# Kernel optimization log

Measured on AMD Instinct MI355X. Metric: run time of the kernel, lower is better.

Reference implementation:

```python
import jax, jax.numpy as jnp
import numpy as np

WS = 7
SHIFT = 3
S_SIZE = 20.0
T_SIZE = 1.0
DIM = 256
HEADS = 8
EPS = 1e-5


def _rel_pos_index(ws):
    coords = np.stack(np.meshgrid(np.arange(ws), np.arange(ws), indexing='ij')).reshape(2, -1)
    rel = (coords[:, :, None] - coords[:, None, :]).transpose(1, 2, 0).copy()
    rel[..., 0] += ws - 1
    rel[..., 1] += ws - 1
    rel[..., 0] *= 2 * ws - 1
    return rel.sum(-1)  # (ws*ws, ws*ws)


def _calc_masks(H, W, ws, shift, s_size, t_size):
    # shifted-window mask (standard Swin)
    img = np.zeros((H, W), dtype=np.float32)
    sl = (slice(0, -ws), slice(-ws, -shift), slice(-shift, None))
    cnt = 0
    for h in sl:
        for w in sl:
            img[h, w] = cnt
            cnt += 1
    N = ws * ws
    mw = img.reshape(H // ws, ws, W // ws, ws).transpose(0, 2, 1, 3).reshape(-1, N)
    am = np.where((mw[:, None, :] - mw[:, :, None]) != 0, -100.0, 0.0).astype(np.float32)
    # physical 'cone' masks
    kmh = 1000.0 / 3600.0
    cv_min, cv_max = 60.0 * kmh, 100.0 * kmh
    cw_min, cw_max = 10.0 * kmh, 25.0 * kmh
    r = np.arange(ws)
    rr, cc = np.meshgrid(r, r, indexing='ij')
    coords = np.stack([rr.ravel(), cc.ravel()], -1)
    delta = coords[:, None, :] - coords[None, :, :]
    dy = delta[..., 0].astype(np.float32) * s_size
    dt = delta[..., 1].astype(np.float32) * t_size
    eye = np.eye(N, dtype=bool)
    dt_pos = dt > 0
    safe_dt = np.where(dt_pos, dt, 1.0)
    sp = np.where(dt_pos, dy / safe_dt, 0.0)
    allow_v = (dt_pos & (dy >= 0) & (sp >= cv_min) & (sp <= cv_max)) | eye
    cone_v = np.where(allow_v, 0.0, -100.0).astype(np.float32)
    spw = np.where(dt_pos, np.abs(dy) / safe_dt, 0.0)
    allow_w = (dt_pos & (dy <= 0) & (spw >= cw_min) & (spw <= cw_max)) | eye
    cone_w = np.where(allow_w, 0.0, -100.0).astype(np.float32)
    return am + cone_v[None], am + cone_w[None]


def _ln(x, g, b):
    mu = jnp.mean(x, -1, keepdims=True)
    var = jnp.mean((x - mu) ** 2, -1, keepdims=True)
    return (x - mu) / jnp.sqrt(var + EPS) * g + b


def _win_part(x, ws):
    B, H, W, C = x.shape
    return x.reshape(B, H // ws, ws, W // ws, ws, C).transpose(0, 1, 3, 2, 4, 5).reshape(-1, ws * ws, C)


def _win_rev(w, ws, H, W):
    B = w.shape[0] // ((H // ws) * (W // ws))
    return w.reshape(B, H // ws, W // ws, ws, ws, -1).transpose(0, 1, 3, 2, 4, 5).reshape(B, H, W, -1)


def _wattn(xw, qkv_w, qkv_b, proj_w, proj_b, rpb, mask, rpi, nH):
    Bw, N, Ch = xw.shape
    hd = Ch // nH
    qkv = (xw @ qkv_w.T + qkv_b).reshape(Bw, N, 3, nH, hd).transpose(2, 0, 3, 1, 4)
    q = qkv[0] * (hd ** -0.5)
    attn = jnp.einsum('bhnd,bhmd->bhnm', q, qkv[1])
    bias = rpb[rpi.reshape(-1)].reshape(N, N, nH).transpose(2, 0, 1)
    attn = attn + bias[None]
    nW = mask.shape[0]
    attn = (attn.reshape(Bw // nW, nW, nH, N, N) + mask[None, :, None]).reshape(Bw, nH, N, N)
    attn = jax.nn.softmax(attn, axis=-1)
    out = jnp.einsum('bhnm,bhmd->bhnd', attn, qkv[2]).transpose(0, 2, 1, 3).reshape(Bw, N, Ch)
    return out @ proj_w.T + proj_b


def _forward(H, W, x, norm1_g, norm1_b, norm2_g, norm2_b,
             qkv_w1, qkv_b1, proj_w1, proj_b1, rpb1,
             qkv_w2, qkv_b2, proj_w2, proj_b2, rpb2,
             fc1_w, fc1_b, fc2_w, fc2_b):
    B, L, C = x.shape
    ws, shift = WS, SHIFT
    m1, m2 = _calc_masks(H, W, ws, shift, S_SIZE, T_SIZE)
    m1, m2 = jnp.asarray(m1), jnp.asarray(m2)
    rpi = jnp.asarray(_rel_pos_index(ws))
    nH = HEADS // 2
    shortcut = x
    xn = _ln(x, norm1_g, norm1_b).reshape(B, H, W, C)
    halves = []
    for xh, qw, qb, pw, pb, rpb, m in (
        (xn[..., :C // 2], qkv_w1, qkv_b1, proj_w1, proj_b1, rpb1, m1),
        (xn[..., C // 2:], qkv_w2, qkv_b2, proj_w2, proj_b2, rpb2, m2),
    ):
        sx = jnp.roll(xh, (-shift, -shift), (1, 2))
        aw = _wattn(_win_part(sx, ws), qw, qb, pw, pb, rpb, m, rpi, nH)
        halves.append(jnp.roll(_win_rev(aw, ws, H, W), (shift, shift), (1, 2)))
    x = shortcut + jnp.concatenate(halves, -1).reshape(B, L, C)
    h = _ln(x, norm2_g, norm2_b)
    h = jax.nn.gelu(h @ fc1_w.T + fc1_b, approximate=False)
    return x + (h @ fc2_w.T + fc2_b)


def setup_inputs() -> dict:
    key = jax.random.key(0)
    B, H, W, C = 2, 224, 224, DIM
    Ch = C // 2
    hid = 4 * C
    nrpb = (2 * WS - 1) * (2 * WS - 1)
    nHh = HEADS // 2
    ks = jax.random.split(key, 16)
    p = lambda k, shape: 0.02 * jax.random.normal(k, shape, dtype=jnp.float32)
    return {
        'x': jax.random.normal(ks[0], (B, H * W, C), dtype=jnp.float32),
        'H': H, 'W': W,
        'norm1_g': jnp.ones((C,), jnp.float32), 'norm1_b': jnp.zeros((C,), jnp.float32),
        'norm2_g': jnp.ones((C,), jnp.float32), 'norm2_b': jnp.zeros((C,), jnp.float32),
        'qkv_w1': p(ks[1], (3 * Ch, Ch)), 'qkv_b1': jnp.zeros((3 * Ch,), jnp.float32),
        'proj_w1': p(ks[2], (Ch, Ch)), 'proj_b1': jnp.zeros((Ch,), jnp.float32),
        'rpb1': p(ks[3], (nrpb, nHh)),
        'qkv_w2': p(ks[4], (3 * Ch, Ch)), 'qkv_b2': jnp.zeros((3 * Ch,), jnp.float32),
        'proj_w2': p(ks[5], (Ch, Ch)), 'proj_b2': jnp.zeros((Ch,), jnp.float32),
        'rpb2': p(ks[6], (nrpb, nHh)),
        'fc1_w': p(ks[7], (hid, C)), 'fc1_b': jnp.zeros((hid,), jnp.float32),
        'fc2_w': p(ks[8], (C, hid)), 'fc2_b': jnp.zeros((C,), jnp.float32),
    }


def reference(x, H, W, norm1_g, norm1_b, norm2_g, norm2_b,
              qkv_w1, qkv_b1, proj_w1, proj_b1, rpb1,
              qkv_w2, qkv_b2, proj_w2, proj_b2, rpb2,
              fc1_w, fc1_b, fc2_w, fc2_b):
    return _forward(H, W, x, norm1_g, norm1_b, norm2_g, norm2_b,
                    qkv_w1, qkv_b1, proj_w1, proj_b1, rpb1,
                    qkv_w2, qkv_b2, proj_w2, proj_b2, rpb2,
                    fc1_w, fc1_b, fc2_w, fc2_b)
```

## Files before the change

### kernel.cpp

```cpp
#include <hip/hip_runtime.h>

using u16 = unsigned short;
typedef short short8 __attribute__((ext_vector_type(8)));
typedef float f32x4 __attribute__((ext_vector_type(4)));

#define T_TOK 100352

__device__ __forceinline__ float bf2f(u16 u) {
    return __uint_as_float(((unsigned int)u) << 16);
}
__device__ __forceinline__ u16 f2bf(float f) {
    unsigned int u = __float_as_uint(f);
    u += 0x7fffu + ((u >> 16) & 1u);
    return (u16)(u >> 16);
}

__global__ __launch_bounds__(256) void cvt_bf16_k(const float* __restrict__ src,
                                                  u16* __restrict__ dst, int n) {
    int i = blockIdx.x * 256 + threadIdx.x;
    int stride = gridDim.x * 256;
    for (; i < n; i += stride) dst[i] = f2bf(src[i]);
}

__global__ __launch_bounds__(256) void bias_tbl_k(const float* __restrict__ rpb0,
                                                  const float* __restrict__ rpb1,
                                                  float* __restrict__ tbl) {
    int id = blockIdx.x;
    int hsel = id >> 4, wtype = (id >> 2) & 3, h = id & 3;
    const float* rpb = hsel ? rpb1 : rpb0;
    int redge = wtype >> 1, cedge = wtype & 1;
    float* o = tbl + (size_t)id * 2401;
    for (int i = threadIdx.x; i < 2401; i += 256) {
        int n = i / 49, m = i - n * 49;
        int rn = n / 7, cn = n - rn * 7, rm = m / 7, cm = m - rm * 7;
        int rpi = (rn - rm + 6) * 13 + (cn - cm + 6);
        float v = rpb[rpi * 4 + h];
        int grn = redge ? (rn < 4 ? 1 : 2) : 0;
        int grm = redge ? (rm < 4 ? 1 : 2) : 0;
        int gcn = cedge ? (cn < 4 ? 1 : 2) : 0;
        int gcm = cedge ? (cm < 4 ? 1 : 2) : 0;
        if ((grn * 3 + gcn) != (grm * 3 + gcm)) v += -100.0f;
        int dr = rn - rm, dc = cn - cm;
        bool ok;
        if (n == m) ok = true;
        else if (hsel == 0)
            ok = (dc == 1 && dr == 1) || (dc == 2 && dr == 2) ||
                 (dc == 3 && (dr == 3 || dr == 4)) ||
                 (dc == 4 && (dr == 4 || dr == 5)) ||
                 (dc == 5 && (dr == 5 || dr == 6)) ||
                 (dc == 6 && (dr == 5 || dr == 6));
        else
            ok = (dr == -1 && dc >= 3 && dc <= 6) || (dr == -2 && dc == 6);
        if (!ok) v += -100.0f;
        o[i] = v;
    }
}

__global__ __launch_bounds__(256) void ln1_k(const float* __restrict__ x,
                                             const float* __restrict__ g,
                                             const float* __restrict__ b,
                                             u16* __restrict__ xw) {
    int t = blockIdx.x * 4 + (threadIdx.x >> 6);
    int lane = threadIdx.x & 63;
    const float4 v = *(const float4*)(x + (size_t)t * 256 + lane * 4);
    float s = v.x + v.y + v.z + v.w;
    float s2 = v.x * v.x + v.y * v.y + v.z * v.z + v.w * v.w;
#pragma unroll
    for (int off = 1; off < 64; off <<= 1) {
        s += __shfl_xor(s, off);
        s2 += __shfl_xor(s2, off);
    }
    float mean = s * (1.0f / 256.0f);
    float var = s2 * (1.0f / 256.0f) - mean * mean;
    float rstd = 1.0f / sqrtf(var + 1e-5f);

    int bb = (t >= 50176) ? 1 : 0;
    int l = t - bb * 50176;
    int rr = l / 224, cc = l - rr * 224;
    int r2 = rr - 3; if (r2 < 0) r2 += 224;
    int c2 = cc - 3; if (c2 < 0) c2 += 224;
    int wi = r2 / 7, lr = r2 - wi * 7;
    int wj = c2 / 7, lc = c2 - wj * 7;
    size_t mIdx = (size_t)(((bb << 10) + wi * 32 + wj) * 49 + lr * 7 + lc);

    int ch = lane * 4;
    int hsel = ch >> 7, colb = ch & 127;
    const float4 gv = *(const float4*)(g + ch);
    const float4 bv = *(const float4*)(b + ch);
    union { uint2 u; u16 s4[4]; } pk;
    pk.s4[0] = f2bf((v.x - mean) * rstd * gv.x + bv.x);
    pk.s4[1] = f2bf((v.y - mean) * rstd * gv.y + bv.y);
    pk.s4[2] = f2bf((v.z - mean) * rstd * gv.z + bv.z);
    pk.s4[3] = f2bf((v.w - mean) * rstd * gv.w + bv.w);
    *(uint2*)(xw + (size_t)hsel * T_TOK * 128 + mIdx * 128 + colb) = pk.u;
}

__global__ __launch_bounds__(256) void ln2_k(const float* __restrict__ x,
                                             const float* __restrict__ g,
                                             const float* __restrict__ b,
                                             u16* __restrict__ h) {
    int t = blockIdx.x * 4 + (threadIdx.x >> 6);
    int lane = threadIdx.x & 63;
    const float4 v = *(const float4*)(x + (size_t)t * 256 + lane * 4);
    float s = v.x + v.y + v.z + v.w;
    float s2 = v.x * v.x + v.y * v.y + v.z * v.z + v.w * v.w;
#pragma unroll
    for (int off = 1; off < 64; off <<= 1) {
        s += __shfl_xor(s, off);
        s2 += __shfl_xor(s2, off);
    }
    float mean = s * (1.0f / 256.0f);
    float var = s2 * (1.0f / 256.0f) - mean * mean;
    float rstd = 1.0f / sqrtf(var + 1e-5f);
    int ch = lane * 4;
    const float4 gv = *(const float4*)(g + ch);
    const float4 bv = *(const float4*)(b + ch);
    union { uint2 u; u16 s4[4]; } pk;
    pk.s4[0] = f2bf((v.x - mean) * rstd * gv.x + bv.x);
    pk.s4[1] = f2bf((v.y - mean) * rstd * gv.y + bv.y);
    pk.s4[2] = f2bf((v.z - mean) * rstd * gv.z + bv.z);
    pk.s4[3] = f2bf((v.w - mean) * rstd * gv.w + bv.w);
    *(uint2*)(h + (size_t)t * 256 + ch) = pk.u;
}

template <int EPI>
__global__ __launch_bounds__(256) void gemm_k(const u16* __restrict__ A,
                                              const u16* __restrict__ W,
                                              const float* __restrict__ bias,
                                              const float* __restrict__ resid,
                                              void* __restrict__ outp,
                                              int K, int hsel) {
    __shared__ u16 As[128][64];
    __shared__ u16 Bs[128][64];
    const int tid = threadIdx.x;
    const int lane = tid & 63;
    const int wave = tid >> 6;
    const int wr = wave >> 1, wc = wave & 1;
    const int bm = blockIdx.x, bn = blockIdx.y;
    const int r = lane & 15, kg = lane >> 4;

    f32x4 acc[4][4] = {};

    for (int kt = 0; kt < K; kt += 64) {
#pragma unroll
        for (int i = 0; i < 4; ++i) {
            int idx = tid + i * 256;
            int row = idx >> 3, cb = idx & 7;
            uint4 va = *(const uint4*)(A + (size_t)(bm * 128 + row) * K + kt + cb * 8);
            *(uint4*)(&As[row][(cb ^ (row & 7)) * 8]) = va;
            uint4 vb = *(const uint4*)(W + (size_t)(bn * 128 + row) * K + kt + cb * 8);
            *(uint4*)(&Bs[row][(cb ^ (row & 7)) * 8]) = vb;
        }
        __syncthreads();
#pragma unroll
        for (int ks = 0; ks < 2; ++ks) {
            short8 fa[4], fb[4];
#pragma unroll
            for (int mf = 0; mf < 4; ++mf) {
                int ra = wr * 64 + mf * 16 + r;
                fa[mf] = *(const short8*)(&As[ra][((ks * 4 + kg) ^ (ra & 7)) * 8]);
            }
#pragma unroll
            for (int nf = 0; nf < 4; ++nf) {
                int rb = wc * 64 + nf * 16 + r;
                fb[nf] = *(const short8*)(&Bs[rb][((ks * 4 + kg) ^ (rb & 7)) * 8]);
            }
#pragma unroll
            for (int mf = 0; mf < 4; ++mf)
#pragma unroll
                for (int nf = 0; nf < 4; ++nf)
                    acc[mf][nf] = __builtin_amdgcn_mfma_f32_16x16x32_bf16(
                        fa[mf], fb[nf], acc[mf][nf], 0, 0, 0);
        }
        __syncthreads();
    }

#pragma unroll
    for (int mf = 0; mf < 4; ++mf) {
#pragma unroll
        for (int nf = 0; nf < 4; ++nf) {
#pragma unroll
            for (int j = 0; j < 4; ++j) {
                int row = wr * 64 + mf * 16 + kg * 4 + j;
                int col = wc * 64 + nf * 16 + r;
                int gm = bm * 128 + row;
                int gn = bn * 128 + col;
                float v = acc[mf][nf][j] + bias[gn];
                if (EPI == 0) {
                    if (gn < 128) v *= 0.17677669529663687f;
                    ((u16*)outp)[(size_t)gm * 384 + gn] = f2bf(v);
                } else if (EPI == 1) {
                    int win = gm / 49, n = gm - win * 49;
                    int bb = win >> 10, w = win & 1023, wi = w >> 5, wj = w & 31;
                    int lr = n / 7, lc = n - lr * 7;
                    int R = wi * 7 + lr + 3;  if (R >= 224) R -= 224;
                    int Cc = wj * 7 + lc + 3; if (Cc >= 224) Cc -= 224;
                    size_t o = ((size_t)bb * 50176 + (size_t)R * 224 + Cc) * 256 +
                               hsel * 128 + gn;
                    ((float*)outp)[o] = resid[o] + v;
                } else if (EPI == 2) {
                    float gl = 0.5f * v * (1.0f + erff(v * 0.70710678118654752f));
                    ((u16*)outp)[(size_t)gm * 1024 + gn] = f2bf(gl);
                } else {
                    size_t o = (size_t)gm * 256 + gn;
                    ((float*)outp)[o] = v + resid[o];
                }
            }
        }
    }
}

__global__ __launch_bounds__(256) void attn_k(const u16* __restrict__ qkv,
                                              const float* __restrict__ btbl,
                                              u16* __restrict__ attnout) {
    int bid = blockIdx.x;
    int hsel = bid >> 11;
    int win = bid & 2047;
    int w = win & 1023;
    int wi = w >> 5, wj = w & 31;
    int wtype = ((wi == 31) ? 2 : 0) + ((wj == 31) ? 1 : 0);
    const u16* src = qkv + (size_t)hsel * T_TOK * 384 + (size_t)win * 49 * 384;

    __shared__ float kv[49][256];
    int tid = threadIdx.x;
    for (int c = tid; c < 1568; c += 256) {
        int row = c >> 5, cc = (c & 31) * 8;
        uint4 u = *(const uint4*)(src + row * 384 + 128 + cc);
        const u16* us = (const u16*)&u;
#pragma unroll
        for (int j = 0; j < 8; ++j) kv[row][cc + j] = bf2f(us[j]);
    }

    int h = tid >> 6, n = tid & 63;
    float q[32];
    bool act = (n < 49);
    if (act) {
        const u16* qp = src + n * 384 + h * 32;
#pragma unroll
        for (int g8 = 0; g8 < 4; ++g8) {
            uint4 u = *(const uint4*)(qp + g8 * 8);
            const u16* us = (const u16*)&u;
#pragma unroll
            for (int j = 0; j < 8; ++j) q[g8 * 8 + j] = bf2f(us[j]);
        }
    }
    __syncthreads();
    if (!act) return;

    const float* bias = btbl + ((size_t)((hsel * 4 + wtype) * 4 + h)) * 2401 + n * 49;
    float o[32];
#pragma unroll
    for (int d = 0; d < 32; ++d) o[d] = 0.0f;
    float sum = 0.0f;

    for (int m = 0; m < 49; ++m) {
        const float4* kr = (const float4*)&kv[m][h * 32];
        float dot = 0.0f;
#pragma unroll
        for (int j = 0; j < 8; ++j) {
            float4 kk = kr[j];
            dot += q[j * 4 + 0] * kk.x + q[j * 4 + 1] * kk.y +
                   q[j * 4 + 2] * kk.z + q[j * 4 + 3] * kk.w;
        }
        float p = __expf(dot + bias[m]);
        sum += p;
        const float4* vr = (const float4*)&kv[m][128 + h * 32];
#pragma unroll
        for (int j = 0; j < 8; ++j) {
            float4 vv = vr[j];
            o[j * 4 + 0] += p * vv.x;
            o[j * 4 + 1] += p * vv.y;
            o[j * 4 + 2] += p * vv.z;
            o[j * 4 + 3] += p * vv.w;
        }
    }
    float inv = 1.0f / sum;
    u16* op = attnout + (size_t)hsel * T_TOK * 128 + (size_t)(win * 49 + n) * 128 + h * 32;
#pragma unroll
    for (int g8 = 0; g8 < 4; ++g8) {
        union { uint4 u; u16 s[8]; } pk;
#pragma unroll
        for (int j = 0; j < 8; ++j) pk.s[j] = f2bf(o[g8 * 8 + j] * inv);
        *(uint4*)(op + g8 * 8) = pk.u;
    }
}

extern "C" void kernel_launch(void* const* d_in, const int* in_sizes, int n_in,
                              void* d_out, int out_size, void* d_ws, size_t ws_size,
                              hipStream_t stream) {
    (void)in_sizes; (void)n_in; (void)out_size; (void)ws_size;
    const float* x      = (const float*)d_in[0];
    const float* n1g    = (const float*)d_in[3];
    const float* n1b    = (const float*)d_in[4];
    const float* n2g    = (const float*)d_in[5];
    const float* n2b    = (const float*)d_in[6];
    const float* qkvw1  = (const float*)d_in[7];
    const float* qkvb1  = (const float*)d_in[8];
    const float* projw1 = (const float*)d_in[9];
    const float* projb1 = (const float*)d_in[10];
    const float* rpb1   = (const float*)d_in[11];
    const float* qkvw2  = (const float*)d_in[12];
    const float* qkvb2  = (const float*)d_in[13];
    const float* projw2 = (const float*)d_in[14];
    const float* projb2 = (const float*)d_in[15];
    const float* rpb2   = (const float*)d_in[16];
    const float* fc1w   = (const float*)d_in[17];
    const float* fc1b   = (const float*)d_in[18];
    const float* fc2w   = (const float*)d_in[19];
    const float* fc2b   = (const float*)d_in[20];
    float* out = (float*)d_out;

    char* ws = (char*)d_ws;
    u16* qkv_buf = (u16*)ws;
    u16* xw      = (u16*)(ws + 154140672LL);
    u16* hidden  = (u16*)ws;
    float* x2    = (float*)(ws + 205520896LL);
    u16* hbuf    = (u16*)(ws + 308281344LL);
    float* btbl  = (float*)(ws + 359661568LL);
    u16* wbf     = (u16*)(ws + 359968896LL);
    u16* qw0 = wbf;
    u16* qw1 = wbf + 49152;
    u16* pw0 = wbf + 98304;
    u16* pw1 = wbf + 114688;
    u16* f1w = wbf + 131072;
    u16* f2w = wbf + 393216;

    cvt_bf16_k<<<48, 256, 0, stream>>>(qkvw1, qw0, 49152);
    cvt_bf16_k<<<48, 256, 0, stream>>>(qkvw2, qw1, 49152);
    cvt_bf16_k<<<16, 256, 0, stream>>>(projw1, pw0, 16384);
    cvt_bf16_k<<<16, 256, 0, stream>>>(projw2, pw1, 16384);
    cvt_bf16_k<<<256, 256, 0, stream>>>(fc1w, f1w, 262144);
    cvt_bf16_k<<<256, 256, 0, stream>>>(fc2w, f2w, 262144);
    bias_tbl_k<<<32, 256, 0, stream>>>(rpb1, rpb2, btbl);

    ln1_k<<<25088, 256, 0, stream>>>(x, n1g, n1b, xw);

    gemm_k<0><<<dim3(784, 3), 256, 0, stream>>>(xw, qw0, qkvb1, nullptr,
                                                qkv_buf, 128, 0);
    gemm_k<0><<<dim3(784, 3), 256, 0, stream>>>(xw + (size_t)T_TOK * 128, qw1, qkvb2,
                                                nullptr, qkv_buf + (size_t)T_TOK * 384,
                                                128, 1);

    attn_k<<<4096, 256, 0, stream>>>(qkv_buf, btbl, xw);

    gemm_k<1><<<dim3(784, 1), 256, 0, stream>>>(xw, pw0, projb1, x, x2, 128, 0);
    gemm_k<1><<<dim3(784, 1), 256, 0, stream>>>(xw + (size_t)T_TOK * 128, pw1, projb2,
                                                x, x2, 128, 1);

    ln2_k<<<25088, 256, 0, stream>>>(x2, n2g, n2b, hbuf);
    gemm_k<2><<<dim3(784, 8), 256, 0, stream>>>(hbuf, f1w, fc1b, nullptr,
                                                hidden, 256, 0);
    gemm_k<3><<<dim3(784, 2), 256, 0, stream>>>(hidden, f2w, fc2b, x2, out, 1024, 0);
}
```

Measured before the change: 792.7 us.

## Use direct global-to-LDS loads in GEMM and tune attention inner loop

The GEMM tile loader now uses global_load_lds 16-byte transfers, so data goes straight from global memory into shared memory without passing through registers. The XOR swizzle moves to the global source address, since the LDS destination is wave-contiguous. The attention kernel gets an occupancy hint of 3 blocks per SM, float4 stores for the bf16-to-float K/V staging, split dot-product accumulators for more ILP, and an unroll-by-7 on the key loop. The 16-byte global_load_lds size and the lane-to-LDS mapping must match the hardware's per-lane layout, or the result will be wrong.

```diff
diff --git a/kernel.cpp b/kernel.cpp
--- a/kernel.cpp
+++ b/kernel.cpp
@@ -13,6 +13,12 @@
     unsigned int u = __float_as_uint(f);
     u += 0x7fffu + ((u >> 16) & 1u);
     return (u16)(u >> 16);
+}
+
+__device__ __forceinline__ void ld_g2l16(const u16* g, u16* l) {
+    __builtin_amdgcn_global_load_lds((const __attribute__((address_space(1))) void*)g,
+                                     (__attribute__((address_space(3))) void*)l,
+                                     16, 0, 0);
 }
 
 __global__ __launch_bounds__(256) void cvt_bf16_k(const float* __restrict__ src,
@@ -138,18 +144,21 @@
     const int wr = wave >> 1, wc = wave & 1;
     const int bm = blockIdx.x, bn = blockIdx.y;
     const int r = lane & 15, kg = lane >> 4;
+    const int wbase = wave * 64;
 
     f32x4 acc[4][4] = {};
 
     for (int kt = 0; kt < K; kt += 64) {
 #pragma unroll
         for (int i = 0; i < 4; ++i) {
-            int idx = tid + i * 256;
-            int row = idx >> 3, cb = idx & 7;
-            uint4 va = *(const uint4*)(A + (size_t)(bm * 128 + row) * K + kt + cb * 8);
-            *(uint4*)(&As[row][(cb ^ (row & 7)) * 8]) = va;
-            uint4 vb = *(const uint4*)(W + (size_t)(bn * 128 + row) * K + kt + cb * 8);
-            *(uint4*)(&Bs[row][(cb ^ (row & 7)) * 8]) = vb;
+            int idx = i * 256 + tid;
+            int row = idx >> 3;
+            int cb = (idx & 7) ^ (row & 7);
+            int ubase = (i * 256 + wbase) * 8;
+            ld_g2l16(A + (size_t)(bm * 128 + row) * K + kt + cb * 8,
+                     &As[0][0] + ubase);
+            ld_g2l16(W + (size_t)(bn * 128 + row) * K + kt + cb * 8,
+                     &Bs[0][0] + ubase);
         }
         __syncthreads();
 #pragma unroll
@@ -210,9 +219,9 @@
     }
 }
 
-__global__ __launch_bounds__(256) void attn_k(const u16* __restrict__ qkv,
-                                              const float* __restrict__ btbl,
-                                              u16* __restrict__ attnout) {
+__global__ __launch_bounds__(256, 3) void attn_k(const u16* __restrict__ qkv,
+                                                 const float* __restrict__ btbl,
+                                                 u16* __restrict__ attnout) {
     int bid = blockIdx.x;
     int hsel = bid >> 11;
     int win = bid & 2047;
@@ -227,8 +236,11 @@
         int row = c >> 5, cc = (c & 31) * 8;
         uint4 u = *(const uint4*)(src + row * 384 + 128 + cc);
         const u16* us = (const u16*)&u;
-#pragma unroll
-        for (int j = 0; j < 8; ++j) kv[row][cc + j] = bf2f(us[j]);
+        float4 f0, f1;
+        f0.x = bf2f(us[0]); f0.y = bf2f(us[1]); f0.z = bf2f(us[2]); f0.w = bf2f(us[3]);
+        f1.x = bf2f(us[4]); f1.y = bf2f(us[5]); f1.z = bf2f(us[6]); f1.w = bf2f(us[7]);
+        *(float4*)(&kv[row][cc]) = f0;
+        *(float4*)(&kv[row][cc + 4]) = f1;
     }
 
     int h = tid >> 6, n = tid & 63;
@@ -253,15 +265,19 @@
     for (int d = 0; d < 32; ++d) o[d] = 0.0f;
     float sum = 0.0f;
 
+#pragma unroll 7
     for (int m = 0; m < 49; ++m) {
         const float4* kr = (const float4*)&kv[m][h * 32];
-        float dot = 0.0f;
-#pragma unroll
-        for (int j = 0; j < 8; ++j) {
-            float4 kk = kr[j];
-            dot += q[j * 4 + 0] * kk.x + q[j * 4 + 1] * kk.y +
-                   q[j * 4 + 2] * kk.z + q[j * 4 + 3] * kk.w;
-        }
+        float d0 = 0.0f, d1 = 0.0f, d2 = 0.0f, d3 = 0.0f;
+#pragma unroll
+        for (int j = 0; j < 8; j += 2) {
+            float4 ka = kr[j], kb = kr[j + 1];
+            d0 += q[j * 4 + 0] * ka.x + q[j * 4 + 4] * kb.x;
+            d1 += q[j * 4 + 1] * ka.y + q[j * 4 + 5] * kb.y;
+            d2 += q[j * 4 + 2] * ka.z + q[j * 4 + 6] * kb.z;
+            d3 += q[j * 4 + 3] * ka.w + q[j * 4 + 7] * kb.w;
+        }
+        float dot = (d0 + d1) + (d2 + d3);
         float p = __expf(dot + bias[m]);
         sum += p;
         const float4* vr = (const float4*)&kv[m][128 + h * 32];
```

New measurement: 826.0 us. 4.2% more time.
